# Optimization experiments

Hardware: AMD Instinct MI355X
Metric: run time of the kernel (lower is better)

The kernel has to match this reference:

```python
import jax, jax.numpy as jnp
import numpy as np

N_NODES = 100_000
N_EDGES = 1_600_000
N_RELS = 16
D_IN = 128
D_OUT = 64


def setup_inputs() -> dict:
    key = jax.random.key(0)
    k_feat, k_w, k_src, k_dst, k_et = jax.random.split(key, 5)
    feat = jax.random.normal(k_feat, (N_NODES, D_IN), dtype=jnp.float32)
    weight = jax.random.normal(k_w, (N_RELS, D_IN, D_OUT), dtype=jnp.float32)
    src = jax.random.randint(k_src, (N_EDGES,), 0, N_NODES, dtype=jnp.int32)
    dst = jax.random.randint(k_dst, (N_EDGES,), 0, N_NODES, dtype=jnp.int32)
    etypes = jnp.sort(jax.random.randint(k_et, (N_EDGES,), 0, N_RELS, dtype=jnp.int32))
    return {"feat": feat, "weight": weight, "src": src, "dst": dst, "etypes": etypes}


def reference(feat, weight, src, dst, etypes):
    # RGCN gather-mm: message m_e = feat[src_e] @ W[etype_e]; out_v = sum_{e: dst_e = v} m_e
    # Efficient form: project all nodes with all relation weights (dense GEMM, small R),
    # then gather the (etype, src) slice per edge and segment-sum into destinations.
    proj = jnp.einsum('nd,rde->rne', feat, weight)          # [R, N, d_out]
    msg = proj[etypes, src]                                  # [E, d_out] irregular gather
    out = jax.ops.segment_sum(msg, dst, num_segments=feat.shape[0])  # [N, d_out] scatter-sum
    return out
```

## Files before the change

### kernel.cpp

```cpp
#include <hip/hip_runtime.h>
#include <hip/hip_bf16.h>


#define NTHREADS 256
#define TM 64
#define CH 2560

typedef __attribute__((ext_vector_type(8))) __bf16 bf16x8;
typedef __attribute__((ext_vector_type(4))) float f32x4;

__global__ void cvt_w_kernel(const float* __restrict__ w,
                             __bf16* __restrict__ o, int total) {
    int idx = blockIdx.x * 256 + threadIdx.x;
    if (idx >= total) return;
    int r = idx >> 13;
    int rem = idx & 8191;
    int k = rem >> 6;
    int n = rem & 63;
    o[(r << 13) + (n << 7) + k] = (__bf16)w[idx];
}

__global__ __launch_bounds__(NTHREADS)
void proj_all_kernel(const float* __restrict__ feat, const __bf16* __restrict__ wtb,
                     const unsigned char* __restrict__ usedb,
                     int N, int R, __bf16* __restrict__ projb) {
    __shared__ __bf16 Wt[2][64 * 136];
    __shared__ unsigned used_l[16 * 32];

    int t = threadIdx.x;
    int wave = t >> 6, lane = t & 63;
    int q = lane >> 4, m = lane & 15;
    long blk0 = (long)blockIdx.x * 128;
    long node0 = blk0 + wave * 32;

    int rpb = (R + 1) >> 1;
    int r0 = blockIdx.y * rpb;
    int r1 = r0 + rpb; if (r1 > R) r1 = R;
    int nr = r1 - r0;
    if (nr <= 0) return;

    for (int c = t; c < nr * 32; c += NTHREADS) {
        int rr = c >> 5, i = c & 31;
        used_l[rr * 32 + i] = *(const unsigned*)(usedb + (size_t)(r0 + rr) * N + blk0 + i * 4);
    }

    bf16x8 a[2][4];
    #pragma unroll
    for (int mt = 0; mt < 2; mt++) {
        long nd = node0 + mt * 16 + m;
        if (nd > N - 1) nd = N - 1;
        const float* arow = feat + nd * 128;
        #pragma unroll
        for (int ks = 0; ks < 4; ks++) {
            float4 fa = *(const float4*)(arow + ks * 32 + q * 8);
            float4 fb = *(const float4*)(arow + ks * 32 + q * 8 + 4);
            bf16x8 v;
            v[0] = (__bf16)fa.x; v[1] = (__bf16)fa.y; v[2] = (__bf16)fa.z; v[3] = (__bf16)fa.w;
            v[4] = (__bf16)fb.x; v[5] = (__bf16)fb.y; v[6] = (__bf16)fb.z; v[7] = (__bf16)fb.w;
            a[mt][ks] = v;
        }
    }

    {
        const __bf16* wg = wtb + ((size_t)r0 << 13);
        #pragma unroll
        for (int i = 0; i < 4; i++) {
            int c = t + i * 256;
            int n = c >> 4, kc = c & 15;
            *(bf16x8*)(&Wt[0][n * 136 + kc * 8]) = *(const bf16x8*)(wg + n * 128 + kc * 8);
        }
    }
    asm volatile("s_waitcnt lgkmcnt(0)" ::: "memory");
    __builtin_amdgcn_s_barrier();
    __builtin_amdgcn_sched_barrier(0);

    for (int ri = 0; ri < nr; ri++) {
        int r = r0 + ri;
        int cur = ri & 1, nxt = cur ^ 1;
        bool pf = (ri + 1 < nr);

        bf16x8 wreg[4];
        if (pf) {
            const __bf16* wg = wtb + ((size_t)(r + 1) << 13);
            #pragma unroll
            for (int i = 0; i < 4; i++) {
                int c = t + i * 256;
                int n = c >> 4, kc = c & 15;
                wreg[i] = *(const bf16x8*)(wg + n * 128 + kc * 8);
            }
        }

        f32x4 acc[2][4] = {};
        #pragma unroll
        for (int ks = 0; ks < 4; ks++) {
            bf16x8 b0 = *(const bf16x8*)(&Wt[cur][(0 * 16 + m) * 136 + ks * 32 + q * 8]);
            bf16x8 b1 = *(const bf16x8*)(&Wt[cur][(1 * 16 + m) * 136 + ks * 32 + q * 8]);
            bf16x8 b2 = *(const bf16x8*)(&Wt[cur][(2 * 16 + m) * 136 + ks * 32 + q * 8]);
            bf16x8 b3 = *(const bf16x8*)(&Wt[cur][(3 * 16 + m) * 136 + ks * 32 + q * 8]);
            #pragma unroll
            for (int mt = 0; mt < 2; mt++) {
                acc[mt][0] = __builtin_amdgcn_mfma_f32_16x16x32_bf16(a[mt][ks], b0, acc[mt][0], 0, 0, 0);
                acc[mt][1] = __builtin_amdgcn_mfma_f32_16x16x32_bf16(a[mt][ks], b1, acc[mt][1], 0, 0, 0);
                acc[mt][2] = __builtin_amdgcn_mfma_f32_16x16x32_bf16(a[mt][ks], b2, acc[mt][2], 0, 0, 0);
                acc[mt][3] = __builtin_amdgcn_mfma_f32_16x16x32_bf16(a[mt][ks], b3, acc[mt][3], 0, 0, 0);
            }
        }

        #pragma unroll
        for (int mt = 0; mt < 2; mt++) {
            unsigned g = used_l[ri * 32 + ((wave * 32 + mt * 16 + q * 4) >> 2)];
            #pragma unroll
            for (int reg = 0; reg < 4; reg++) {
                long nd = node0 + mt * 16 + q * 4 + reg;
                if (nd < N && ((g >> (reg * 8)) & 1)) {
                    union { unsigned long long u; __bf16 h[4]; } pk;
                    pk.h[0] = (__bf16)acc[mt][0][reg];
                    pk.h[1] = (__bf16)acc[mt][1][reg];
                    pk.h[2] = (__bf16)acc[mt][2][reg];
                    pk.h[3] = (__bf16)acc[mt][3][reg];
                    *(unsigned long long*)(projb + ((size_t)r * N + nd) * 64 + m * 4) = pk.u;
                }
            }
        }

        if (pf) {
            #pragma unroll
            for (int i = 0; i < 4; i++) {
                int c = t + i * 256;
                int n = c >> 4, kc = c & 15;
                *(bf16x8*)(&Wt[nxt][n * 136 + kc * 8]) = wreg[i];
            }
            asm volatile("s_waitcnt lgkmcnt(0)" ::: "memory");
            __builtin_amdgcn_s_barrier();
            __builtin_amdgcn_sched_barrier(0);
        }
    }
}

__global__ __launch_bounds__(1024)
void bucket_scatter(const int* __restrict__ dst, const int* __restrict__ src,
                    const int* __restrict__ etypes, int E, int N, int NB, int STRIDE,
                    int* __restrict__ bcnt, int* __restrict__ items,
                    unsigned char* __restrict__ usedb) {
    __shared__ int lh[1024], lb[1024];
    int t = threadIdx.x;
    lh[t] = 0;
    __syncthreads();
    long base = (long)blockIdx.x * 8192;
    int bs[8], it[8];
    #pragma unroll
    for (int i = 0; i < 8; i++) {
        long e = base + t + 1024 * i;
        if (e < E) {
            int d = dst[e];
            int bkt = d >> 7;
            bs[i] = bkt;
            int pair = etypes[e] * N + src[e];
            it[i] = ((d & 127) << 24) | pair;
            usedb[pair] = 1;
            atomicAdd(&lh[bkt], 1);
        } else bs[i] = -1;
    }
    __syncthreads();
    for (int bb = t; bb < NB; bb += 1024) {
        int c = lh[bb];
        lb[bb] = c ? atomicAdd(&bcnt[bb], c) : 0;
        lh[bb] = 0;
    }
    __syncthreads();
    #pragma unroll
    for (int i = 0; i < 8; i++) {
        if (bs[i] >= 0) {
            int pos = lb[bs[i]] + atomicAdd(&lh[bs[i]], 1);
            if (pos < STRIDE)
                items[(size_t)bs[i] * STRIDE + pos] = it[i];
        }
    }
}

__global__ __launch_bounds__(512)
void bucket_reduce(const int* __restrict__ bcnt, const int* __restrict__ items,
                   int STRIDE, const __bf16* __restrict__ projb, int N,
                   float* __restrict__ out) {
    __shared__ int h[128], sc[128], cur[128];
    __shared__ int its[CH];
    int b = blockIdx.x, t = threadIdx.x;
    int cnt = bcnt[b]; if (cnt > STRIDE) cnt = STRIDE;
    const int* bitems = items + (size_t)b * STRIDE;
    int sub = t >> 3, c8 = t & 7;

    float acc[2][8] = {};

    for (int c0 = 0; c0 < cnt; c0 += CH) {
        int n = cnt - c0; if (n > CH) n = CH;

        if (t < 128) h[t] = 0;
        __syncthreads();

        int my[CH / 512];
        int dl[CH / 512];
        #pragma unroll
        for (int i = 0; i < CH / 512; i++) {
            int k = t + i * 512;
            if (k < n) {
                my[i] = bitems[c0 + k];
                dl[i] = ((unsigned)my[i]) >> 24;
                atomicAdd(&h[dl[i]], 1);
            } else dl[i] = -1;
        }
        __syncthreads();

        if (t < 128) sc[t] = h[t];
        __syncthreads();
        for (int s = 1; s < 128; s <<= 1) {
            int add = (t >= s && t < 128) ? sc[t - s] : 0;
            __syncthreads();
            if (t < 128) sc[t] += add;
            __syncthreads();
        }
        if (t < 128) cur[t] = sc[t] - h[t];
        __syncthreads();

        #pragma unroll
        for (int i = 0; i < CH / 512; i++) {
            if (dl[i] >= 0) {
                int pos = atomicAdd(&cur[dl[i]], 1);
                its[pos] = my[i] & 0xFFFFFF;
            }
        }
        __syncthreads();

        #pragma unroll
        for (int idx = 0; idx < 2; idx++) {
            int d = sub + idx * 64;
            int s = sc[d] - h[d];
            int e = sc[d];
            int k = s;
            for (; k + 1 < e; k += 2) {
                int p0 = its[k], p1 = its[k + 1];
                bf16x8 v0 = *(const bf16x8*)(projb + (size_t)p0 * 64 + c8 * 8);
                bf16x8 v1 = *(const bf16x8*)(projb + (size_t)p1 * 64 + c8 * 8);
                #pragma unroll
                for (int i = 0; i < 8; i++) acc[idx][i] += (float)v0[i] + (float)v1[i];
            }
            if (k < e) {
                int p = its[k];
                bf16x8 v0 = *(const bf16x8*)(projb + (size_t)p * 64 + c8 * 8);
                #pragma unroll
                for (int i = 0; i < 8; i++) acc[idx][i] += (float)v0[i];
            }
        }
        __syncthreads();
    }

    #pragma unroll
    for (int idx = 0; idx < 2; idx++) {
        long v = (long)b * 128 + sub + idx * 64;
        if (v < N) {
            float* orow = out + (size_t)v * 64;
            #pragma unroll
            for (int i = 0; i < 8; i++) {
                int cp = c8 * 8 + i;
                orow[(cp & 3) * 16 + (cp >> 2)] = acc[idx][i];
            }
        }
    }
}

__global__ __launch_bounds__(NTHREADS)
void rgcn_atomic(const float* __restrict__ feat, const float* __restrict__ weight,
                 const int* __restrict__ src, const int* __restrict__ dst,
                 const int* __restrict__ etypes, int E,
                 float* __restrict__ out) {
    __shared__ __bf16 Wt[64 * 136];
    int b = blockIdx.x;
    int e0 = b * TM;
    int t = threadIdx.x;
    int wave = t >> 6, lane = t & 63;
    int q = lane >> 4, m = lane & 15;
    int wbase = e0 + wave * 16;
    int last = e0 + TM - 1; if (last > E - 1) last = E - 1;
    int rmin = etypes[e0];
    int rmax = etypes[last];
    int em = wbase + m;
    bool rowok = em < E;
    int ei = rowok ? em : E - 1;
    int my_et = rowok ? etypes[em] : -1;
    const float* arow = feat + (long)src[ei] * 128;
    bf16x8 a[4];
    #pragma unroll
    for (int ks = 0; ks < 4; ks++) {
        float4 fa = *(const float4*)(arow + ks * 32 + q * 8);
        float4 fb = *(const float4*)(arow + ks * 32 + q * 8 + 4);
        bf16x8 v;
        v[0] = (__bf16)fa.x; v[1] = (__bf16)fa.y;
        v[2] = (__bf16)fa.z; v[3] = (__bf16)fa.w;
        v[4] = (__bf16)fb.x; v[5] = (__bf16)fb.y;
        v[6] = (__bf16)fb.z; v[7] = (__bf16)fb.w;
        a[ks] = v;
    }
    f32x4 acc0 = {0.f, 0.f, 0.f, 0.f};
    f32x4 acc1 = {0.f, 0.f, 0.f, 0.f};
    f32x4 acc2 = {0.f, 0.f, 0.f, 0.f};
    f32x4 acc3 = {0.f, 0.f, 0.f, 0.f};
    for (int r = rmin; r <= rmax; ++r) {
        if (r != rmin) __syncthreads();
        const float* wg = weight + (r << 13);
        for (int p = t; p < 4096; p += NTHREADS) {
            int n = p & 63, kh = p >> 6;
            float w0 = wg[(kh * 2) * 64 + n];
            float w1 = wg[(kh * 2 + 1) * 64 + n];
            union { unsigned u; __bf16 h[2]; } pk;
            pk.h[0] = (__bf16)w0; pk.h[1] = (__bf16)w1;
            *(unsigned*)&Wt[n * 136 + kh * 2] = pk.u;
        }
        __syncthreads();
        bool on = (my_et == r);
        #pragma unroll
        for (int ks = 0; ks < 4; ks++) {
            bf16x8 af = a[ks];
            if (!on) {
                #pragma unroll
                for (int j = 0; j < 8; j++) af[j] = (__bf16)0.f;
            }
            bf16x8 b0 = *(const bf16x8*)(&Wt[(0 * 16 + m) * 136 + ks * 32 + q * 8]);
            bf16x8 b1 = *(const bf16x8*)(&Wt[(1 * 16 + m) * 136 + ks * 32 + q * 8]);
            bf16x8 b2 = *(const bf16x8*)(&Wt[(2 * 16 + m) * 136 + ks * 32 + q * 8]);
            bf16x8 b3 = *(const bf16x8*)(&Wt[(3 * 16 + m) * 136 + ks * 32 + q * 8]);
            acc0 = __builtin_amdgcn_mfma_f32_16x16x32_bf16(af, b0, acc0, 0, 0, 0);
            acc1 = __builtin_amdgcn_mfma_f32_16x16x32_bf16(af, b1, acc1, 0, 0, 0);
            acc2 = __builtin_amdgcn_mfma_f32_16x16x32_bf16(af, b2, acc2, 0, 0, 0);
            acc3 = __builtin_amdgcn_mfma_f32_16x16x32_bf16(af, b3, acc3, 0, 0, 0);
        }
    }
    #pragma unroll
    for (int reg = 0; reg < 4; reg++) {
        int er = wbase + q * 4 + reg;
        if (er < E) {
            float* orow = out + (long)dst[er] * 64;
            unsafeAtomicAdd(orow + 0 * 16 + m, acc0[reg]);
            unsafeAtomicAdd(orow + 1 * 16 + m, acc1[reg]);
            unsafeAtomicAdd(orow + 2 * 16 + m, acc2[reg]);
            unsafeAtomicAdd(orow + 3 * 16 + m, acc3[reg]);
        }
    }
}

extern "C" void kernel_launch(void* const* d_in, const int* in_sizes, int n_in,
                              void* d_out, int out_size, void* d_ws, size_t ws_size,
                              hipStream_t stream) {
    const float* feat   = (const float*)d_in[0];
    const float* weight = (const float*)d_in[1];
    const int*   src    = (const int*)d_in[2];
    const int*   dst    = (const int*)d_in[3];
    const int*   etypes = (const int*)d_in[4];
    float* out = (float*)d_out;

    int nfeat = in_sizes[0];
    int nw    = in_sizes[1];
    int E     = in_sizes[2];
    int N     = nfeat / 128;
    int R     = nw >> 13;
    int NB    = (N + 127) >> 7;

    int avg = (int)(((long)E + NB - 1) / NB);
    int STRIDE = ((avg * 2 + 63) / 64) * 64;
    if (STRIDE < 1024) STRIDE = 1024;

    size_t o = 0;
    auto take = [&](size_t bytes) { size_t r = o; o = (o + bytes + 255) & ~(size_t)255; return r; };
    size_t o_bcnt  = take((size_t)NB * 4);
    size_t o_usedb = take((size_t)R * N);
    size_t o_items = take((size_t)NB * STRIDE * 4);
    size_t o_wtb   = take((size_t)nw * 2);
    size_t o_projb = take((size_t)R * N * 64 * 2);
    size_t need = o;

    bool fast = (ws_size >= need) && (NB <= 1024) && ((size_t)R * N < (1u << 24)) && (R <= 16);

    if (fast) {
        char* ws = (char*)d_ws;
        int* bcnt  = (int*)(ws + o_bcnt);
        unsigned char* usedb = (unsigned char*)(ws + o_usedb);
        int* items = (int*)(ws + o_items);
        __bf16* wtb   = (__bf16*)(ws + o_wtb);
        __bf16* projb = (__bf16*)(ws + o_projb);

        int cgrid = (int)(((long)E + 8191) / 8192);

        hipMemsetAsync(bcnt, 0, (o_usedb - o_bcnt) + (size_t)R * N, stream);
        bucket_scatter<<<cgrid, 1024, 0, stream>>>(dst, src, etypes, E, N, NB, STRIDE,
                                                   bcnt, items, usedb);
        cvt_w_kernel<<<(nw + 255) / 256, 256, 0, stream>>>(weight, wtb, nw);

        dim3 pgrid((N + 127) / 128, 2);
        proj_all_kernel<<<pgrid, NTHREADS, 0, stream>>>(feat, wtb, usedb, N, R, projb);
        bucket_reduce<<<NB, 512, 0, stream>>>(bcnt, items, STRIDE, projb, N, out);
    } else {
        hipMemsetAsync(d_out, 0, (size_t)out_size * sizeof(float), stream);
        int mgrid = (E + TM - 1) / TM;
        rgcn_atomic<<<mgrid, NTHREADS, 0, stream>>>(feat, weight, src, dst, etypes, E, out);
    }
}
```

Baseline: 237.3 us.

## Fuse all stages into one cooperative persistent kernel with grid syncs

Replaces the memset, bucket scatter, weight conversion, projection and bucket reduce launches with a single cooperative kernel that separates the phases with grid.sync barriers. This removes per-launch overhead and inter-kernel gaps. The cost is that occupancy is capped at the co-resident grid size, each phase uses 512-thread blocks, and every grid-wide barrier waits for the slowest block. The old multi-kernel path is kept as a fallback if the cooperative launch is unavailable or fails.

```diff
diff --git a/kernel.cpp b/kernel.cpp
--- a/kernel.cpp
+++ b/kernel.cpp
@@ -1,5 +1,8 @@
 #include <hip/hip_runtime.h>
 #include <hip/hip_bf16.h>
+#include <hip/hip_cooperative_groups.h>
+
+namespace cg = cooperative_groups;
 
 
 #define NTHREADS 256
@@ -8,6 +11,308 @@
 
 typedef __attribute__((ext_vector_type(8))) __bf16 bf16x8;
 typedef __attribute__((ext_vector_type(4))) float f32x4;
+
+__global__ __launch_bounds__(512, 4)
+void mega_kernel(const float* __restrict__ feat, const float* __restrict__ weight,
+                 const int* __restrict__ src, const int* __restrict__ dst,
+                 const int* __restrict__ etypes,
+                 int E, int N, int R, int NB, int STRIDE,
+                 int* __restrict__ bcnt, int* __restrict__ items,
+                 unsigned char* __restrict__ usedb,
+                 __bf16* __restrict__ wtb, __bf16* __restrict__ projb,
+                 float* __restrict__ out) {
+    cg::grid_group grid = cg::this_grid();
+    __shared__ __attribute__((aligned(16))) char smem[36864];
+
+    int t = threadIdx.x;
+    int bid = blockIdx.x;
+    int nb = gridDim.x;
+    long gtid = (long)bid * 512 + t;
+    long gthreads = (long)nb * 512;
+
+    for (long i = gtid; i < NB; i += gthreads) bcnt[i] = 0;
+    long ub4 = ((long)R * N) >> 2;
+    unsigned* usedw = (unsigned*)usedb;
+    for (long i = gtid; i < ub4; i += gthreads) usedw[i] = 0;
+    long nwtot = (long)R << 13;
+    for (long i = gtid; i < nwtot; i += gthreads) {
+        int r = (int)(i >> 13);
+        int rem = (int)(i & 8191);
+        int k = rem >> 6, n = rem & 63;
+        wtb[((size_t)r << 13) + (n << 7) + k] = (__bf16)weight[i];
+    }
+    __threadfence();
+    grid.sync();
+
+    {
+        int* lh = (int*)smem;
+        int* lb = ((int*)smem) + 1024;
+        int nchunk = (int)(((long)E + 2047) / 2048);
+        for (int ch = bid; ch < nchunk; ch += nb) {
+            for (int i = t; i < 1024; i += 512) lh[i] = 0;
+            __syncthreads();
+            long base = (long)ch * 2048;
+            int bs[4], it[4];
+            #pragma unroll
+            for (int i = 0; i < 4; i++) {
+                long e = base + t + 512 * i;
+                if (e < E) {
+                    int d = dst[e];
+                    int bkt = d >> 7;
+                    bs[i] = bkt;
+                    int pair = etypes[e] * N + src[e];
+                    it[i] = ((d & 127) << 24) | pair;
+                    usedb[pair] = 1;
+                    atomicAdd(&lh[bkt], 1);
+                } else bs[i] = -1;
+            }
+            __syncthreads();
+            for (int bb = t; bb < NB; bb += 512) {
+                int c = lh[bb];
+                lb[bb] = c ? atomicAdd(&bcnt[bb], c) : 0;
+                lh[bb] = 0;
+            }
+            __syncthreads();
+            #pragma unroll
+            for (int i = 0; i < 4; i++) {
+                if (bs[i] >= 0) {
+                    int pos = lb[bs[i]] + atomicAdd(&lh[bs[i]], 1);
+                    if (pos < STRIDE)
+                        items[(size_t)bs[i] * STRIDE + pos] = it[i];
+                }
+            }
+            __syncthreads();
+        }
+    }
+    __threadfence();
+    grid.sync();
+
+    {
+        __bf16* Wt0 = (__bf16*)smem;
+        __bf16* Wt1 = ((__bf16*)smem) + 64 * 136;
+        unsigned* used_l = (unsigned*)(smem + 34816);
+
+        int wave = t >> 6;
+        int half = wave >> 2;
+        int w4 = wave & 3;
+        int lane = t & 63;
+        int q = lane >> 4, m = lane & 15;
+
+        int PT = (N + 127) / 128;
+        int TP = (PT + 1) >> 1;
+        int rpb = (R + 1) >> 1;
+        int nslice = TP * 2;
+
+        for (int s = bid; s < nslice; s += nb) {
+            __syncthreads();
+            int pair = s >> 1, rh = s & 1;
+            int tile = pair * 2 + half;
+            bool tileok = tile < PT;
+            int r0 = rh * rpb;
+            int r1 = r0 + rpb; if (r1 > R) r1 = R;
+            int nr = r1 - r0;
+            if (nr <= 0) continue;
+
+            long blk0 = (long)tile * 128;
+            long node0 = blk0 + w4 * 32;
+
+            {
+                int hh = t >> 8, rem = t & 255;
+                int rr = rem >> 5, i = rem & 31;
+                int th = pair * 2 + hh;
+                if (rr < nr && th < PT)
+                    used_l[t] = *(const unsigned*)(usedb + (size_t)(r0 + rr) * N + (long)th * 128 + i * 4);
+            }
+
+            bf16x8 a[2][4];
+            #pragma unroll
+            for (int mt = 0; mt < 2; mt++) {
+                long nd = node0 + mt * 16 + m;
+                if (!tileok || nd > N - 1) nd = N - 1;
+                const float* arow = feat + nd * 128;
+                #pragma unroll
+                for (int ks = 0; ks < 4; ks++) {
+                    float4 fa = *(const float4*)(arow + ks * 32 + q * 8);
+                    float4 fb = *(const float4*)(arow + ks * 32 + q * 8 + 4);
+                    bf16x8 v;
+                    v[0] = (__bf16)fa.x; v[1] = (__bf16)fa.y; v[2] = (__bf16)fa.z; v[3] = (__bf16)fa.w;
+                    v[4] = (__bf16)fb.x; v[5] = (__bf16)fb.y; v[6] = (__bf16)fb.z; v[7] = (__bf16)fb.w;
+                    a[mt][ks] = v;
+                }
+            }
+
+            {
+                const __bf16* wg = wtb + ((size_t)r0 << 13);
+                #pragma unroll
+                for (int i = 0; i < 2; i++) {
+                    int c = t + i * 512;
+                    int n = c >> 4, kc = c & 15;
+                    *(bf16x8*)(&Wt0[n * 136 + kc * 8]) = *(const bf16x8*)(wg + n * 128 + kc * 8);
+                }
+            }
+            asm volatile("s_waitcnt lgkmcnt(0)" ::: "memory");
+            __builtin_amdgcn_s_barrier();
+            __builtin_amdgcn_sched_barrier(0);
+
+            for (int ri = 0; ri < nr; ri++) {
+                int r = r0 + ri;
+                __bf16* Wcur = (ri & 1) ? Wt1 : Wt0;
+                __bf16* Wnxt = (ri & 1) ? Wt0 : Wt1;
+                bool pf = (ri + 1 < nr);
+
+                bf16x8 wreg[2];
+                if (pf) {
+                    const __bf16* wg = wtb + ((size_t)(r + 1) << 13);
+                    #pragma unroll
+                    for (int i = 0; i < 2; i++) {
+                        int c = t + i * 512;
+                        int n = c >> 4, kc = c & 15;
+                        wreg[i] = *(const bf16x8*)(wg + n * 128 + kc * 8);
+                    }
+                }
+
+                f32x4 acc[2][4] = {};
+                #pragma unroll
+                for (int ks = 0; ks < 4; ks++) {
+                    bf16x8 b0 = *(const bf16x8*)(&Wcur[(0 * 16 + m) * 136 + ks * 32 + q * 8]);
+                    bf16x8 b1 = *(const bf16x8*)(&Wcur[(1 * 16 + m) * 136 + ks * 32 + q * 8]);
+                    bf16x8 b2 = *(const bf16x8*)(&Wcur[(2 * 16 + m) * 136 + ks * 32 + q * 8]);
+                    bf16x8 b3 = *(const bf16x8*)(&Wcur[(3 * 16 + m) * 136 + ks * 32 + q * 8]);
+                    #pragma unroll
+                    for (int mt = 0; mt < 2; mt++) {
+                        acc[mt][0] = __builtin_amdgcn_mfma_f32_16x16x32_bf16(a[mt][ks], b0, acc[mt][0], 0, 0, 0);
+                        acc[mt][1] = __builtin_amdgcn_mfma_f32_16x16x32_bf16(a[mt][ks], b1, acc[mt][1], 0, 0, 0);
+                        acc[mt][2] = __builtin_amdgcn_mfma_f32_16x16x32_bf16(a[mt][ks], b2, acc[mt][2], 0, 0, 0);
+                        acc[mt][3] = __builtin_amdgcn_mfma_f32_16x16x32_bf16(a[mt][ks], b3, acc[mt][3], 0, 0, 0);
+                    }
+                }
+
+                #pragma unroll
+                for (int mt = 0; mt < 2; mt++) {
+                    unsigned g = used_l[half * 256 + ri * 32 + ((w4 * 32 + mt * 16 + q * 4) >> 2)];
+                    #pragma unroll
+                    for (int reg = 0; reg < 4; reg++) {
+                        long nd = node0 + mt * 16 + q * 4 + reg;
+                        if (tileok && nd < N && ((g >> (reg * 8)) & 1)) {
+                            union { unsigned long long u; __bf16 h[4]; } pk;
+                            pk.h[0] = (__bf16)acc[mt][0][reg];
+                            pk.h[1] = (__bf16)acc[mt][1][reg];
+                            pk.h[2] = (__bf16)acc[mt][2][reg];
+                            pk.h[3] = (__bf16)acc[mt][3][reg];
+                            *(unsigned long long*)(projb + ((size_t)r * N + nd) * 64 + m * 4) = pk.u;
+                        }
+                    }
+                }
+
+                if (pf) {
+                    #pragma unroll
+                    for (int i = 0; i < 2; i++) {
+                        int c = t + i * 512;
+                        int n = c >> 4, kc = c & 15;
+                        *(bf16x8*)(&Wnxt[n * 136 + kc * 8]) = wreg[i];
+                    }
+                    asm volatile("s_waitcnt lgkmcnt(0)" ::: "memory");
+                    __builtin_amdgcn_s_barrier();
+                    __builtin_amdgcn_sched_barrier(0);
+                }
+            }
+        }
+    }
+    __threadfence();
+    grid.sync();
+
+    {
+        int* h   = (int*)smem;
+        int* sc_ = ((int*)smem) + 128;
+        int* cur = ((int*)smem) + 256;
+        int* its = ((int*)smem) + 384;
+        int sub = t >> 3, c8 = t & 7;
+
+        for (int b = bid; b < NB; b += nb) {
+            __syncthreads();
+            int cnt = bcnt[b]; if (cnt > STRIDE) cnt = STRIDE;
+            const int* bitems = items + (size_t)b * STRIDE;
+
+            float acc[2][8] = {};
+
+            for (int c0 = 0; c0 < cnt; c0 += CH) {
+                int n = cnt - c0; if (n > CH) n = CH;
+
+                if (t < 128) h[t] = 0;
+                __syncthreads();
+
+                int my[CH / 512];
+                int dl[CH / 512];
+                #pragma unroll
+                for (int i = 0; i < CH / 512; i++) {
+                    int k = t + i * 512;
+                    if (k < n) {
+                        my[i] = bitems[c0 + k];
+                        dl[i] = ((unsigned)my[i]) >> 24;
+                        atomicAdd(&h[dl[i]], 1);
+                    } else dl[i] = -1;
+                }
+                __syncthreads();
+
+                if (t < 128) sc_[t] = h[t];
+                __syncthreads();
+                for (int s = 1; s < 128; s <<= 1) {
+                    int add = (t >= s && t < 128) ? sc_[t - s] : 0;
+                    __syncthreads();
+                    if (t < 128) sc_[t] += add;
+                    __syncthreads();
+                }
+                if (t < 128) cur[t] = sc_[t] - h[t];
+                __syncthreads();
+
+                #pragma unroll
+                for (int i = 0; i < CH / 512; i++) {
+                    if (dl[i] >= 0) {
+                        int pos = atomicAdd(&cur[dl[i]], 1);
+                        its[pos] = my[i] & 0xFFFFFF;
+                    }
+                }
+                __syncthreads();
+
+                #pragma unroll
+                for (int idx = 0; idx < 2; idx++) {
+                    int d = sub + idx * 64;
+                    int s0 = sc_[d] - h[d];
+                    int e0 = sc_[d];
+                    int k = s0;
+                    for (; k + 1 < e0; k += 2) {
+                        int p0 = its[k], p1 = its[k + 1];
+                        bf16x8 v0 = *(const bf16x8*)(projb + (size_t)p0 * 64 + c8 * 8);
+                        bf16x8 v1 = *(const bf16x8*)(projb + (size_t)p1 * 64 + c8 * 8);
+                        #pragma unroll
+                        for (int i = 0; i < 8; i++) acc[idx][i] += (float)v0[i] + (float)v1[i];
+                    }
+                    if (k < e0) {
+                        int p = its[k];
+                        bf16x8 v0 = *(const bf16x8*)(projb + (size_t)p * 64 + c8 * 8);
+                        #pragma unroll
+                        for (int i = 0; i < 8; i++) acc[idx][i] += (float)v0[i];
+                    }
+                }
+                __syncthreads();
+            }
+
+            #pragma unroll
+            for (int idx = 0; idx < 2; idx++) {
+                long v = (long)b * 128 + sub + idx * 64;
+                if (v < N) {
+                    float* orow = out + (size_t)v * 64;
+                    #pragma unroll
+                    for (int i = 0; i < 8; i++) {
+                        int cp = c8 * 8 + i;
+                        orow[(cp & 3) * 16 + (cp >> 2)] = acc[idx][i];
+                    }
+                }
+            }
+        }
+    }
+}
+
 
 __global__ void cvt_w_kernel(const float* __restrict__ w,
                              __bf16* __restrict__ o, int total) {
@@ -376,7 +681,8 @@
     size_t o_projb = take((size_t)R * N * 64 * 2);
     size_t need = o;
 
-    bool fast = (ws_size >= need) && (NB <= 1024) && ((size_t)R * N < (1u << 24)) && (R <= 16);
+    bool fast = (ws_size >= need) && (NB <= 1024) && ((size_t)R * N < (1u << 24))
+                && (R <= 16) && ((N & 3) == 0);
 
     if (fast) {
         char* ws = (char*)d_ws;
@@ -386,13 +692,42 @@
         __bf16* wtb   = (__bf16*)(ws + o_wtb);
         __bf16* projb = (__bf16*)(ws + o_projb);
 
+        static int coopBlocks = -2;
+        if (coopBlocks == -2) {
+            int supportsCoop = 0;
+            if (hipDeviceGetAttribute(&supportsCoop, hipDeviceAttributeCooperativeLaunch, 0) != hipSuccess)
+                supportsCoop = 0;
+            int bpc = 0;
+            if (supportsCoop &&
+                hipOccupancyMaxActiveBlocksPerMultiprocessor(&bpc, mega_kernel, 512, 0) != hipSuccess)
+                bpc = 0;
+            hipDeviceProp_t prop;
+            int ncu = 0;
+            if (hipGetDeviceProperties(&prop, 0) == hipSuccess) ncu = prop.multiProcessorCount;
+            coopBlocks = (supportsCoop && bpc > 0 && ncu > 0) ? bpc * ncu : 0;
+        }
+
+        if (coopBlocks > 0) {
+            const float* a_feat = feat; const float* a_weight = weight;
+            const int* a_src = src; const int* a_dst = dst; const int* a_et = etypes;
+            int a_E = E, a_N = N, a_R = R, a_NB = NB, a_S = STRIDE;
+            int* a_bcnt = bcnt; int* a_items = items;
+            unsigned char* a_usedb = usedb;
+            __bf16* a_wtb = wtb; __bf16* a_projb = projb;
+            float* a_out = out;
+            void* args[] = { &a_feat, &a_weight, &a_src, &a_dst, &a_et,
+                             &a_E, &a_N, &a_R, &a_NB, &a_S,
+                             &a_bcnt, &a_items, &a_usedb, &a_wtb, &a_projb, &a_out };
+            hipError_t err = hipLaunchCooperativeKernel(mega_kernel,
+                                 dim3(coopBlocks), dim3(512), args, 0, stream);
+            if (err == hipSuccess) return;
+        }
+
         int cgrid = (int)(((long)E + 8191) / 8192);
-
-        hipMemsetAsync(bcnt, 0, (o_usedb - o_bcnt) + (size_t)R * N, stream);
+        hipMemsetAsync(bcnt, 0, (o_items - o_bcnt), stream);
         bucket_scatter<<<cgrid, 1024, 0, stream>>>(dst, src, etypes, E, N, NB, STRIDE,
                                                    bcnt, items, usedb);
         cvt_w_kernel<<<(nw + 255) / 256, 256, 0, stream>>>(weight, wtb, nw);
-
         dim3 pgrid((N + 127) / 128, 2);
         proj_all_kernel<<<pgrid, NTHREADS, 0, stream>>>(feat, wtb, usedb, N, R, projb);
         bucket_reduce<<<NB, 512, 0, stream>>>(bcnt, items, STRIDE, projb, N, out);
```

After: 524.0 us. 121% more time.
